# Performance work log

Hardware: AMD Instinct MI355X
Metric: run time of the kernel (lower is better)

Reference implementation:

```python
import jax, jax.numpy as jnp
import numpy as np

N_NODES = 50000
IN_CH, HID_CH, OUT_CH = 128, 128, 64
N_EDGES = 800000


def setup_inputs() -> dict:
    key = jax.random.key(0)
    k = jax.random.split(key, 6)
    x = jax.random.normal(k[0], (N_NODES, IN_CH), dtype=jnp.float32)
    edge_index = jax.random.randint(k[1], (2, N_EDGES), 0, N_NODES, dtype=jnp.int64)
    # Glorot-ish init for weights
    W1 = jax.random.normal(k[2], (IN_CH, HID_CH), dtype=jnp.float32) * (1.0 / np.sqrt(IN_CH))
    b1 = jnp.zeros((HID_CH,), dtype=jnp.float32)
    W2 = jax.random.normal(k[3], (HID_CH, OUT_CH), dtype=jnp.float32) * (1.0 / np.sqrt(HID_CH))
    b2 = jnp.zeros((OUT_CH,), dtype=jnp.float32)
    return {"x": x, "edge_index": edge_index, "W1": W1, "b1": b1, "W2": W2, "b2": b2}


def _gcn_conv(x, src, dst, W, b, n_nodes):
    """PyG GCNConv: linear, add self-loops, symmetric deg^-1/2 normalization, scatter-add."""
    h = x @ W  # [N, F_out]
    loop = jnp.arange(n_nodes, dtype=src.dtype)
    s = jnp.concatenate([src, loop])  # [E+N]
    d = jnp.concatenate([dst, loop])
    # in-degree on target nodes (including self-loops), edge weight = 1
    deg = jnp.zeros((n_nodes,), dtype=h.dtype).at[d].add(1.0)
    dinv = jnp.where(deg > 0, jax.lax.rsqrt(deg), 0.0)
    norm = dinv[s] * dinv[d]  # [E+N]
    msg = h[s] * norm[:, None]  # [E+N, F_out]
    out = jax.ops.segment_sum(msg, d, num_segments=n_nodes)
    return out + b


def reference(x, edge_index, W1, b1, W2, b2):
    src, dst = edge_index[0], edge_index[1]
    h = _gcn_conv(x, src, dst, W1, b1, N_NODES)
    h = jax.nn.relu(h)
    # dropout in eval mode -> identity
    out = _gcn_conv(h, src, dst, W2, b2, N_NODES)
    return out
```

## Files before the change

kernel.cpp:

```cpp
#include <hip/hip_runtime.h>

typedef __attribute__((ext_vector_type(8))) short bf16x8;
typedef __attribute__((ext_vector_type(4))) float f32x4;

constexpr int NN = 50000;
constexpr int NE = 800000;
constexpr int C1 = 128;
constexpr int C2 = 64;
constexpr int NBK = 196;
constexpr int EPB = 2048;
constexpr int NBLK = (NE + EPB - 1) / EPB;
constexpr int MT = NN / 16;
constexpr int MMB = 500;
constexpr int MMWAVES = MMB * 4;
constexpr int CAP = 8192;
constexpr int GB = (NN + 3) / 4;

__device__ __forceinline__ unsigned short f2bf(float f) {
    unsigned int u = __float_as_uint(f);
    u += 0x7FFFu + ((u >> 16) & 1u);
    return (unsigned short)(u >> 16);
}
__device__ __forceinline__ float2 bf2f(unsigned int u) {
    return make_float2(__uint_as_float(u << 16), __uint_as_float(u & 0xFFFF0000u));
}
__device__ __forceinline__ bf16x8 pack8(float4 a, float4 b) {
    bf16x8 r;
    r[0] = (short)f2bf(a.x); r[1] = (short)f2bf(a.y);
    r[2] = (short)f2bf(a.z); r[3] = (short)f2bf(a.w);
    r[4] = (short)f2bf(b.x); r[5] = (short)f2bf(b.y);
    r[6] = (short)f2bf(b.z); r[7] = (short)f2bf(b.w);
    return r;
}

__global__ __launch_bounds__(256) void bin_kernel(const int* __restrict__ src,
                                                  const int* __restrict__ dst,
                                                  unsigned int* __restrict__ ebuf,
                                                  int* __restrict__ localOff) {
    __shared__ int lhist[NBK];
    __shared__ int ls[256];
    __shared__ int lcur[NBK];
    __shared__ unsigned int lbuf[EPB];
    const int t = threadIdx.x;
    const int base = blockIdx.x * EPB;
    if (t < NBK) lhist[t] = 0;
    __syncthreads();
    int b[8]; unsigned int p[8];
    #pragma unroll
    for (int i = 0; i < 8; i++) {
        int e = base + i * 256 + t;
        if (e < NE) {
            int s = src[e], d = dst[e];
            b[i] = d >> 8;
            p[i] = ((unsigned int)(d & 255) << 16) | (unsigned int)s;
            atomicAdd(&lhist[b[i]], 1);
        } else b[i] = -1;
    }
    __syncthreads();
    int v = (t < NBK) ? lhist[t] : 0;
    ls[t] = v;
    __syncthreads();
    #pragma unroll
    for (int d = 1; d < 256; d <<= 1) {
        int u = (t >= d) ? ls[t - d] : 0;
        __syncthreads();
        ls[t] += u;
        __syncthreads();
    }
    if (t < NBK) {
        lcur[t] = ls[t] - v;
        localOff[blockIdx.x * 200 + t] = ls[t] - v;
    }
    if (t == NBK - 1) localOff[blockIdx.x * 200 + NBK] = ls[t];
    __syncthreads();
    #pragma unroll
    for (int i = 0; i < 8; i++) {
        if (b[i] >= 0) {
            int lp = atomicAdd(&lcur[b[i]], 1);
            lbuf[lp] = p[i];
        }
    }
    __syncthreads();
    #pragma unroll
    for (int i = 0; i < 8; i++)
        ebuf[base + i * 256 + t] = lbuf[i * 256 + t];
}

__global__ __launch_bounds__(256) void place_kernel(const unsigned int* __restrict__ ebuf,
                                                    const int* __restrict__ localOff,
                                                    unsigned short* __restrict__ esrc,
                                                    int* __restrict__ cnt,
                                                    int* __restrict__ off,
                                                    float* __restrict__ dinv) {
    __shared__ unsigned int lbuf[CAP];
    __shared__ int lhist[256];
    __shared__ int ls[256];
    __shared__ int lcur[256];
    __shared__ int red[256];
    const int t = threadIdx.x;
    const int bkt = blockIdx.x;
    const int node0 = bkt << 8;
    const int nnodes = min(256, NN - node0);

    const int j0 = 2 * t, j1 = 2 * t + 1;
    int s0 = 0, l0 = 0, s1 = 0, l1 = 0;
    if (j0 < NBLK) { s0 = localOff[j0 * 200 + bkt]; l0 = localOff[j0 * 200 + bkt + 1] - s0; }
    if (j1 < NBLK) { s1 = localOff[j1 * 200 + bkt]; l1 = localOff[j1 * 200 + bkt + 1] - s1; }

    red[t] = s0 + s1;
    ls[t] = l0 + l1;
    lhist[t] = 0;
    __syncthreads();
    #pragma unroll
    for (int d = 1; d < 256; d <<= 1) {
        int u = (t >= d) ? ls[t - d] : 0;
        int r = (t + d < 256) ? red[t + d] : 0;
        __syncthreads();
        ls[t] += u;
        red[t] += r;
        __syncthreads();
    }
    const int segBase = red[0];
    const int total = ls[255];
    const int base0 = ls[t] - (l0 + l1);
    const int base1 = base0 + l0;
    const bool fits = (total <= CAP);

    if (fits) {
        const unsigned int* q0 = ebuf + j0 * EPB + s0;
        for (int k = 0; k < l0; k++) lbuf[base0 + k] = q0[k];
        const unsigned int* q1 = ebuf + j1 * EPB + s1;
        for (int k = 0; k < l1; k++) lbuf[base1 + k] = q1[k];
        __syncthreads();
        for (int k = t; k < total; k += 256) atomicAdd(&lhist[lbuf[k] >> 16], 1);
    } else {
        const unsigned int* q0 = ebuf + j0 * EPB + s0;
        for (int k = 0; k < l0; k++) atomicAdd(&lhist[q0[k] >> 16], 1);
        const unsigned int* q1 = ebuf + j1 * EPB + s1;
        for (int k = 0; k < l1; k++) atomicAdd(&lhist[q1[k] >> 16], 1);
    }
    __syncthreads();
    int v = lhist[t];
    ls[t] = v;
    __syncthreads();
    #pragma unroll
    for (int d = 1; d < 256; d <<= 1) {
        int u = (t >= d) ? ls[t - d] : 0;
        __syncthreads();
        ls[t] += u;
        __syncthreads();
    }
    int ex = ls[t] - v;
    lcur[t] = ex;
    if (t < nnodes) {
        cnt[node0 + t] = v;
        off[node0 + t] = segBase + ex;
        dinv[node0 + t] = rsqrtf((float)v + 1.0f);
    }
    __syncthreads();
    if (fits) {
        for (int k = t; k < total; k += 256) {
            unsigned int pp = lbuf[k];
            int lp = atomicAdd(&lcur[pp >> 16], 1);
            esrc[segBase + lp] = (unsigned short)(pp & 0xFFFFu);
        }
    } else {
        const unsigned int* q0 = ebuf + j0 * EPB + s0;
        for (int k = 0; k < l0; k++) {
            unsigned int pp = q0[k];
            int lp = atomicAdd(&lcur[pp >> 16], 1);
            esrc[segBase + lp] = (unsigned short)(pp & 0xFFFFu);
        }
        const unsigned int* q1 = ebuf + j1 * EPB + s1;
        for (int k = 0; k < l1; k++) {
            unsigned int pp = q1[k];
            int lp = atomicAdd(&lcur[pp >> 16], 1);
            esrc[segBase + lp] = (unsigned short)(pp & 0xFFFFu);
        }
    }
}

__global__ __launch_bounds__(256, 2) void mm1_kernel(const float* __restrict__ x,
                                                     const float* __restrict__ W,
                                                     const float* __restrict__ dinv,
                                                     unsigned short* __restrict__ g1) {
    __shared__ unsigned short wl[4][8][64][8];
    const int t = threadIdx.x;
    for (int i = 0; i < 64; i++) {
        int idx = i * 256 + t;
        int k = idx >> 7, n = idx & 127;
        wl[k >> 5][n >> 4][((k >> 3) & 3) * 16 + (n & 15)][k & 7] = f2bf(W[idx]);
    }
    __syncthreads();
    const int lane = t & 63, lm = lane & 15, quad = lane >> 4;

    bf16x8 bfr[4][8];
    #pragma unroll
    for (int s = 0; s < 4; s++)
        #pragma unroll
        for (int nt = 0; nt < 8; nt++)
            bfr[s][nt] = *(const bf16x8*)&wl[s][nt][lane][0];

    int wg = blockIdx.x * 4 + (t >> 6);
    for (int tile = wg; tile < MT; tile += MMWAVES) {
        int row0 = tile << 4;
        const float* xr = x + (size_t)(row0 + lm) * 128 + quad * 8;
        bf16x8 af[4];
        #pragma unroll
        for (int s = 0; s < 4; s++) {
            float4 p = *(const float4*)(xr + s * 32);
            float4 q = *(const float4*)(xr + s * 32 + 4);
            af[s] = pack8(p, q);
        }
        f32x4 acc[8];
        #pragma unroll
        for (int nt = 0; nt < 8; nt++) acc[nt] = (f32x4){0.f, 0.f, 0.f, 0.f};
        #pragma unroll
        for (int s = 0; s < 4; s++)
            #pragma unroll
            for (int nt = 0; nt < 8; nt++)
                acc[nt] = __builtin_amdgcn_mfma_f32_16x16x32_bf16(af[s], bfr[s][nt],
                                                                  acc[nt], 0, 0, 0);
        float4 dv = *(const float4*)(dinv + row0 + quad * 4);
        float dvv[4] = {dv.x, dv.y, dv.z, dv.w};
        #pragma unroll
        for (int nt = 0; nt < 8; nt++)
            #pragma unroll
            for (int r = 0; r < 4; r++)
                g1[(size_t)(row0 + quad * 4 + r) * 128 + nt * 16 + lm] =
                    f2bf(acc[nt][r] * dvv[r]);
    }
}

__global__ __launch_bounds__(256, 2) void mm2_kernel(const unsigned short* __restrict__ x2,
                                                     const float* __restrict__ W,
                                                     const float* __restrict__ dinv,
                                                     unsigned short* __restrict__ g2) {
    __shared__ unsigned short wl[4][4][64][8];
    const int t = threadIdx.x;
    for (int i = 0; i < 32; i++) {
        int idx = i * 256 + t;
        int k = idx >> 6, n = idx & 63;
        wl[k >> 5][n >> 4][((k >> 3) & 3) * 16 + (n & 15)][k & 7] = f2bf(W[idx]);
    }
    __syncthreads();
    const int lane = t & 63, lm = lane & 15, quad = lane >> 4;

    bf16x8 bfr[4][4];
    #pragma unroll
    for (int s = 0; s < 4; s++)
        #pragma unroll
        for (int nt = 0; nt < 4; nt++)
            bfr[s][nt] = *(const bf16x8*)&wl[s][nt][lane][0];

    int wg = blockIdx.x * 4 + (t >> 6);
    for (int tile = wg; tile < MT; tile += MMWAVES) {
        int row0 = tile << 4;
        const bf16x8* xr = (const bf16x8*)(x2 + (size_t)(row0 + lm) * 128 + quad * 8);
        bf16x8 af[4];
        #pragma unroll
        for (int s = 0; s < 4; s++) af[s] = xr[s * 4];
        f32x4 acc[4];
        #pragma unroll
        for (int nt = 0; nt < 4; nt++) acc[nt] = (f32x4){0.f, 0.f, 0.f, 0.f};
        #pragma unroll
        for (int s = 0; s < 4; s++)
            #pragma unroll
            for (int nt = 0; nt < 4; nt++)
                acc[nt] = __builtin_amdgcn_mfma_f32_16x16x32_bf16(af[s], bfr[s][nt],
                                                                  acc[nt], 0, 0, 0);
        float4 dv = *(const float4*)(dinv + row0 + quad * 4);
        float dvv[4] = {dv.x, dv.y, dv.z, dv.w};
        #pragma unroll
        for (int nt = 0; nt < 4; nt++)
            #pragma unroll
            for (int r = 0; r < 4; r++)
                g2[(size_t)(row0 + quad * 4 + r) * 64 + nt * 16 + lm] =
                    f2bf(acc[nt][r] * dvv[r]);
    }
}

__global__ __launch_bounds__(256) void gather1_kernel(const unsigned short* __restrict__ g1,
                                                      const unsigned short* __restrict__ esrc,
                                                      const int* __restrict__ off,
                                                      const int* __restrict__ cnt,
                                                      const float* __restrict__ dinv,
                                                      const float* __restrict__ b1,
                                                      unsigned short* __restrict__ x2) {
    const int n = blockIdx.x * 4 + (threadIdx.x >> 6);
    if (n >= NN) return;
    const int lane = threadIdx.x & 63;
    const unsigned int* G = (const unsigned int*)g1;
    float2 ps = bf2f(G[(size_t)n * 64 + lane]);
    float a0 = ps.x, a1 = ps.y;
    float c0 = 0.f, c1 = 0.f;
    const int s0 = off[n], c = cnt[n];
    for (int base = 0; base < c; base += 64) {
        const int m = min(64, c - base);
        int vidx = 0;
        if (lane < m) vidx = esrc[s0 + base + lane];
        int i = 0;
        for (; i + 3 < m; i += 4) {
            int sA = __shfl(vidx, i);
            int sB = __shfl(vidx, i + 1);
            int sC = __shfl(vidx, i + 2);
            int sD = __shfl(vidx, i + 3);
            unsigned int vA = G[(size_t)sA * 64 + lane];
            unsigned int vB = G[(size_t)sB * 64 + lane];
            unsigned int vC = G[(size_t)sC * 64 + lane];
            unsigned int vD = G[(size_t)sD * 64 + lane];
            float2 pA = bf2f(vA); a0 += pA.x; a1 += pA.y;
            float2 pB = bf2f(vB); c0 += pB.x; c1 += pB.y;
            float2 pC = bf2f(vC); a0 += pC.x; a1 += pC.y;
            float2 pD = bf2f(vD); c0 += pD.x; c1 += pD.y;
        }
        for (; i < m; i++) {
            int sA = __shfl(vidx, i);
            float2 pA = bf2f(G[(size_t)sA * 64 + lane]);
            a0 += pA.x; a1 += pA.y;
        }
    }
    a0 += c0; a1 += c1;
    const float sc = dinv[n];
    const float2 bb = ((const float2*)b1)[lane];
    const float o0 = fmaxf(sc * a0 + bb.x, 0.f);
    const float o1 = fmaxf(sc * a1 + bb.y, 0.f);
    const unsigned int uo = (unsigned int)f2bf(o0) | ((unsigned int)f2bf(o1) << 16);
    ((unsigned int*)x2)[(size_t)n * 64 + lane] = uo;
}

__global__ __launch_bounds__(256) void gather2_kernel(const unsigned short* __restrict__ g2,
                                                      const unsigned short* __restrict__ esrc,
                                                      const int* __restrict__ off,
                                                      const int* __restrict__ cnt,
                                                      const float* __restrict__ dinv,
                                                      const float* __restrict__ b2,
                                                      float* __restrict__ out) {
    const int n = blockIdx.x * 4 + (threadIdx.x >> 6);
    if (n >= NN) return;
    const int lane = threadIdx.x & 63;
    const unsigned short* G = g2;
    float a0 = __uint_as_float((unsigned int)G[(size_t)n * 64 + lane] << 16);
    float c0 = 0.f;
    const int s0 = off[n], c = cnt[n];
    for (int base = 0; base < c; base += 64) {
        const int m = min(64, c - base);
        int vidx = 0;
        if (lane < m) vidx = esrc[s0 + base + lane];
        int i = 0;
        for (; i + 3 < m; i += 4) {
            int sA = __shfl(vidx, i);
            int sB = __shfl(vidx, i + 1);
            int sC = __shfl(vidx, i + 2);
            int sD = __shfl(vidx, i + 3);
            unsigned short vA = G[(size_t)sA * 64 + lane];
            unsigned short vB = G[(size_t)sB * 64 + lane];
            unsigned short vC = G[(size_t)sC * 64 + lane];
            unsigned short vD = G[(size_t)sD * 64 + lane];
            a0 += __uint_as_float((unsigned int)vA << 16);
            c0 += __uint_as_float((unsigned int)vB << 16);
            a0 += __uint_as_float((unsigned int)vC << 16);
            c0 += __uint_as_float((unsigned int)vD << 16);
        }
        for (; i < m; i++) {
            int sA = __shfl(vidx, i);
            a0 += __uint_as_float((unsigned int)G[(size_t)sA * 64 + lane] << 16);
        }
    }
    a0 += c0;
    const float sc = dinv[n];
    out[(size_t)n * 64 + lane] = sc * a0 + b2[lane];
}

extern "C" void kernel_launch(void* const* d_in, const int* in_sizes, int n_in,
                              void* d_out, int out_size, void* d_ws, size_t ws_size,
                              hipStream_t stream) {
    const float* x  = (const float*)d_in[0];
    const int* edges = (const int*)d_in[1];
    const float* W1 = (const float*)d_in[2];
    const float* b1 = (const float*)d_in[3];
    const float* W2 = (const float*)d_in[4];
    const float* b2 = (const float*)d_in[5];
    const int* src = edges;
    const int* dst = edges + NE;

    int* localOff  = (int*)d_ws;
    unsigned int* ebuf = (unsigned int*)(localOff + 78208);
    unsigned short* esrc = (unsigned short*)(ebuf + (size_t)NBLK * EPB);
    int* cnt       = (int*)(esrc + 800768);
    int* off       = cnt + 50048;
    float* dinv    = (float*)(off + 50048);
    unsigned short* g1 = (unsigned short*)(dinv + 50048);
    unsigned short* x2 = g1 + (size_t)NN * C1;
    unsigned short* g2 = g1;
    float* out = (float*)d_out;

    bin_kernel<<<NBLK, 256, 0, stream>>>(src, dst, ebuf, localOff);
    place_kernel<<<NBK, 256, 0, stream>>>(ebuf, localOff, esrc, cnt, off, dinv);

    mm1_kernel<<<MMB, 256, 0, stream>>>(x, W1, dinv, g1);
    gather1_kernel<<<GB, 256, 0, stream>>>(g1, esrc, off, cnt, dinv, b1, x2);

    mm2_kernel<<<MMB, 256, 0, stream>>>(x2, W2, dinv, g2);
    gather2_kernel<<<GB, 256, 0, stream>>>(g2, esrc, off, cnt, dinv, b2, out);
}
```

Baseline: 182.8 us.

## Fuse edge binning with first matmul and gather1 with second matmul

The edge-binning kernel and the first dense matmul now run as one horizontally fused launch, with block index deciding the role, so the matmul no longer waits for binning. The dinv row scaling of g1 moves into place_kernel, which rescales its bucket's rows after computing degrees. The first-layer gather, bias and ReLU are fused with the second matmul: each block aggregates 16 rows into shared memory and feeds them straight to MFMA, which avoids writing and rereading the x2 intermediate and drops two launches. The cost is an extra read-modify-write pass over g1 and less gather parallelism per block in the fused kernel.

```diff
diff --git a/kernel.cpp b/kernel.cpp
--- a/kernel.cpp
+++ b/kernel.cpp
@@ -11,10 +11,12 @@
 constexpr int EPB = 2048;
 constexpr int NBLK = (NE + EPB - 1) / EPB;
 constexpr int MT = NN / 16;
-constexpr int MMB = 500;
-constexpr int MMWAVES = MMB * 4;
 constexpr int CAP = 8192;
 constexpr int GB = (NN + 3) / 4;
+
+constexpr int K1G = 1024;
+constexpr int MM1_NW = (K1G - NBLK) * 4;
+constexpr int K3G = 1792;
 
 __device__ __forceinline__ unsigned short f2bf(float f) {
     unsigned int u = __float_as_uint(f);
@@ -23,6 +25,9 @@
 }
 __device__ __forceinline__ float2 bf2f(unsigned int u) {
     return make_float2(__uint_as_float(u << 16), __uint_as_float(u & 0xFFFF0000u));
+}
+__device__ __forceinline__ unsigned int pk2(float a, float b) {
+    return (unsigned int)f2bf(a) | ((unsigned int)f2bf(b) << 16);
 }
 __device__ __forceinline__ bf16x8 pack8(float4 a, float4 b) {
     bf16x8 r;
@@ -33,17 +38,19 @@
     return r;
 }
 
-__global__ __launch_bounds__(256) void bin_kernel(const int* __restrict__ src,
-                                                  const int* __restrict__ dst,
-                                                  unsigned int* __restrict__ ebuf,
-                                                  int* __restrict__ localOff) {
-    __shared__ int lhist[NBK];
-    __shared__ int ls[256];
-    __shared__ int lcur[NBK];
-    __shared__ unsigned int lbuf[EPB];
+struct BinSmem {
+    int lhist[NBK];
+    int ls[256];
+    int lcur[NBK];
+    unsigned int lbuf[EPB];
+};
+
+__device__ void bin_work(const int* __restrict__ src, const int* __restrict__ dst,
+                         unsigned int* __restrict__ ebuf, int* __restrict__ localOff,
+                         BinSmem& S) {
     const int t = threadIdx.x;
     const int base = blockIdx.x * EPB;
-    if (t < NBK) lhist[t] = 0;
+    if (t < NBK) S.lhist[t] = 0;
     __syncthreads();
     int b[8]; unsigned int p[8];
     #pragma unroll
@@ -53,37 +60,96 @@
             int s = src[e], d = dst[e];
             b[i] = d >> 8;
             p[i] = ((unsigned int)(d & 255) << 16) | (unsigned int)s;
-            atomicAdd(&lhist[b[i]], 1);
+            atomicAdd(&S.lhist[b[i]], 1);
         } else b[i] = -1;
     }
     __syncthreads();
-    int v = (t < NBK) ? lhist[t] : 0;
-    ls[t] = v;
+    int v = (t < NBK) ? S.lhist[t] : 0;
+    S.ls[t] = v;
     __syncthreads();
     #pragma unroll
     for (int d = 1; d < 256; d <<= 1) {
-        int u = (t >= d) ? ls[t - d] : 0;
-        __syncthreads();
-        ls[t] += u;
+        int u = (t >= d) ? S.ls[t - d] : 0;
+        __syncthreads();
+        S.ls[t] += u;
         __syncthreads();
     }
     if (t < NBK) {
-        lcur[t] = ls[t] - v;
-        localOff[blockIdx.x * 200 + t] = ls[t] - v;
-    }
-    if (t == NBK - 1) localOff[blockIdx.x * 200 + NBK] = ls[t];
+        S.lcur[t] = S.ls[t] - v;
+        localOff[blockIdx.x * 200 + t] = S.ls[t] - v;
+    }
+    if (t == NBK - 1) localOff[blockIdx.x * 200 + NBK] = S.ls[t];
     __syncthreads();
     #pragma unroll
     for (int i = 0; i < 8; i++) {
         if (b[i] >= 0) {
-            int lp = atomicAdd(&lcur[b[i]], 1);
-            lbuf[lp] = p[i];
+            int lp = atomicAdd(&S.lcur[b[i]], 1);
+            S.lbuf[lp] = p[i];
         }
     }
     __syncthreads();
     #pragma unroll
     for (int i = 0; i < 8; i++)
-        ebuf[base + i * 256 + t] = lbuf[i * 256 + t];
+        ebuf[base + i * 256 + t] = S.lbuf[i * 256 + t];
+}
+
+__device__ void mm1_work(const float* __restrict__ x, const float* __restrict__ W,
+                         unsigned short* __restrict__ g1,
+                         unsigned short (&wl)[4][8][64][8]) {
+    const int t = threadIdx.x;
+    for (int i = 0; i < 64; i++) {
+        int idx = i * 256 + t;
+        int k = idx >> 7, n = idx & 127;
+        wl[k >> 5][n >> 4][((k >> 3) & 3) * 16 + (n & 15)][k & 7] = f2bf(W[idx]);
+    }
+    __syncthreads();
+    const int lane = t & 63, lm = lane & 15, quad = lane >> 4;
+
+    bf16x8 bfr[4][8];
+    #pragma unroll
+    for (int s = 0; s < 4; s++)
+        #pragma unroll
+        for (int nt = 0; nt < 8; nt++)
+            bfr[s][nt] = *(const bf16x8*)&wl[s][nt][lane][0];
+
+    const int widx = (blockIdx.x - NBLK) * 4 + (t >> 6);
+    for (int tile = widx; tile < MT; tile += MM1_NW) {
+        int row0 = tile << 4;
+        const float* xr = x + (size_t)(row0 + lm) * 128 + quad * 8;
+        bf16x8 af[4];
+        #pragma unroll
+        for (int s = 0; s < 4; s++) {
+            float4 p = *(const float4*)(xr + s * 32);
+            float4 q = *(const float4*)(xr + s * 32 + 4);
+            af[s] = pack8(p, q);
+        }
+        f32x4 acc[8];
+        #pragma unroll
+        for (int nt = 0; nt < 8; nt++) acc[nt] = (f32x4){0.f, 0.f, 0.f, 0.f};
+        #pragma unroll
+        for (int s = 0; s < 4; s++)
+            #pragma unroll
+            for (int nt = 0; nt < 8; nt++)
+                acc[nt] = __builtin_amdgcn_mfma_f32_16x16x32_bf16(af[s], bfr[s][nt],
+                                                                  acc[nt], 0, 0, 0);
+        #pragma unroll
+        for (int nt = 0; nt < 8; nt++)
+            #pragma unroll
+            for (int r = 0; r < 4; r++)
+                g1[(size_t)(row0 + quad * 4 + r) * 128 + nt * 16 + lm] = f2bf(acc[nt][r]);
+    }
+}
+
+__global__ __launch_bounds__(256, 2) void k1_kernel(const int* __restrict__ src,
+                                                    const int* __restrict__ dst,
+                                                    unsigned int* __restrict__ ebuf,
+                                                    int* __restrict__ localOff,
+                                                    const float* __restrict__ x,
+                                                    const float* __restrict__ W1,
+                                                    unsigned short* __restrict__ g1) {
+    __shared__ union { BinSmem b; unsigned short wl[4][8][64][8]; } sm;
+    if (blockIdx.x < NBLK) bin_work(src, dst, ebuf, localOff, sm.b);
+    else                   mm1_work(x, W1, g1, sm.wl);
 }
 
 __global__ __launch_bounds__(256) void place_kernel(const unsigned int* __restrict__ ebuf,
@@ -91,7 +157,8 @@
                                                     unsigned short* __restrict__ esrc,
                                                     int* __restrict__ cnt,
                                                     int* __restrict__ off,
-                                                    float* __restrict__ dinv) {
+                                                    float* __restrict__ dinv,
+                                                    unsigned short* __restrict__ g1) {
     __shared__ unsigned int lbuf[CAP];
     __shared__ int lhist[256];
     __shared__ int ls[256];
@@ -178,155 +245,92 @@
             esrc[segBase + lp] = (unsigned short)(pp & 0xFFFFu);
         }
     }
-}
-
-__global__ __launch_bounds__(256, 2) void mm1_kernel(const float* __restrict__ x,
-                                                     const float* __restrict__ W,
-                                                     const float* __restrict__ dinv,
-                                                     unsigned short* __restrict__ g1) {
-    __shared__ unsigned short wl[4][8][64][8];
-    const int t = threadIdx.x;
-    for (int i = 0; i < 64; i++) {
-        int idx = i * 256 + t;
-        int k = idx >> 7, n = idx & 127;
-        wl[k >> 5][n >> 4][((k >> 3) & 3) * 16 + (n & 15)][k & 7] = f2bf(W[idx]);
-    }
-    __syncthreads();
-    const int lane = t & 63, lm = lane & 15, quad = lane >> 4;
-
-    bf16x8 bfr[4][8];
-    #pragma unroll
-    for (int s = 0; s < 4; s++)
-        #pragma unroll
-        for (int nt = 0; nt < 8; nt++)
-            bfr[s][nt] = *(const bf16x8*)&wl[s][nt][lane][0];
-
-    int wg = blockIdx.x * 4 + (t >> 6);
-    for (int tile = wg; tile < MT; tile += MMWAVES) {
-        int row0 = tile << 4;
-        const float* xr = x + (size_t)(row0 + lm) * 128 + quad * 8;
-        bf16x8 af[4];
-        #pragma unroll
-        for (int s = 0; s < 4; s++) {
-            float4 p = *(const float4*)(xr + s * 32);
-            float4 q = *(const float4*)(xr + s * 32 + 4);
-            af[s] = pack8(p, q);
-        }
-        f32x4 acc[8];
-        #pragma unroll
-        for (int nt = 0; nt < 8; nt++) acc[nt] = (f32x4){0.f, 0.f, 0.f, 0.f};
-        #pragma unroll
-        for (int s = 0; s < 4; s++)
-            #pragma unroll
-            for (int nt = 0; nt < 8; nt++)
-                acc[nt] = __builtin_amdgcn_mfma_f32_16x16x32_bf16(af[s], bfr[s][nt],
-                                                                  acc[nt], 0, 0, 0);
-        float4 dv = *(const float4*)(dinv + row0 + quad * 4);
-        float dvv[4] = {dv.x, dv.y, dv.z, dv.w};
-        #pragma unroll
-        for (int nt = 0; nt < 8; nt++)
-            #pragma unroll
-            for (int r = 0; r < 4; r++)
-                g1[(size_t)(row0 + quad * 4 + r) * 128 + nt * 16 + lm] =
-                    f2bf(acc[nt][r] * dvv[r]);
-    }
-}
-
-__global__ __launch_bounds__(256, 2) void mm2_kernel(const unsigned short* __restrict__ x2,
-                                                     const float* __restrict__ W,
-                                                     const float* __restrict__ dinv,
-                                                     unsigned short* __restrict__ g2) {
-    __shared__ unsigned short wl[4][4][64][8];
+    const int w = t >> 6, lane = t & 63;
+    unsigned int* g1u = (unsigned int*)g1;
+    for (int r = w; r < nnodes; r += 4) {
+        const float dn = dinv[node0 + r];
+        const size_t a = (size_t)(node0 + r) * 64 + lane;
+        float2 p = bf2f(g1u[a]);
+        g1u[a] = pk2(dn * p.x, dn * p.y);
+    }
+}
+
+__global__ __launch_bounds__(256) void gmm_kernel(const unsigned short* __restrict__ g1,
+                                                  const unsigned short* __restrict__ esrc,
+                                                  const int* __restrict__ off,
+                                                  const int* __restrict__ cnt,
+                                                  const float* __restrict__ dinv,
+                                                  const float* __restrict__ b1,
+                                                  const float* __restrict__ W2,
+                                                  unsigned short* __restrict__ g2) {
+    __shared__ unsigned short wl2[4][4][64][8];
+    __shared__ unsigned short x2t[16][136];
     const int t = threadIdx.x;
     for (int i = 0; i < 32; i++) {
         int idx = i * 256 + t;
         int k = idx >> 6, n = idx & 63;
-        wl[k >> 5][n >> 4][((k >> 3) & 3) * 16 + (n & 15)][k & 7] = f2bf(W[idx]);
-    }
-    __syncthreads();
-    const int lane = t & 63, lm = lane & 15, quad = lane >> 4;
-
-    bf16x8 bfr[4][4];
-    #pragma unroll
-    for (int s = 0; s < 4; s++)
-        #pragma unroll
-        for (int nt = 0; nt < 4; nt++)
-            bfr[s][nt] = *(const bf16x8*)&wl[s][nt][lane][0];
-
-    int wg = blockIdx.x * 4 + (t >> 6);
-    for (int tile = wg; tile < MT; tile += MMWAVES) {
-        int row0 = tile << 4;
-        const bf16x8* xr = (const bf16x8*)(x2 + (size_t)(row0 + lm) * 128 + quad * 8);
+        wl2[k >> 5][n >> 4][((k >> 3) & 3) * 16 + (n & 15)][k & 7] = f2bf(W2[idx]);
+    }
+    const int lane = t & 63, w = t >> 6, lm = lane & 15, quad = lane >> 4;
+    const unsigned int* G = (const unsigned int*)g1;
+    const float2 bb = ((const float2*)b1)[lane];
+
+    for (int tile = blockIdx.x; tile < MT; tile += K3G) {
+        __syncthreads();
+        #pragma unroll 1
+        for (int k4 = 0; k4 < 4; k4++) {
+            const int n = tile * 16 + w * 4 + k4;
+            float2 ps = bf2f(G[(size_t)n * 64 + lane]);
+            float a0 = ps.x, a1 = ps.y;
+            float c0 = 0.f, c1 = 0.f;
+            const int s0 = off[n], c = cnt[n];
+            for (int base = 0; base < c; base += 64) {
+                const int m = min(64, c - base);
+                int vidx = 0;
+                if (lane < m) vidx = esrc[s0 + base + lane];
+                int i = 0;
+                for (; i + 3 < m; i += 4) {
+                    int sA = __shfl(vidx, i),     sB = __shfl(vidx, i + 1);
+                    int sC = __shfl(vidx, i + 2), sD = __shfl(vidx, i + 3);
+                    unsigned int vA = G[(size_t)sA * 64 + lane];
+                    unsigned int vB = G[(size_t)sB * 64 + lane];
+                    unsigned int vC = G[(size_t)sC * 64 + lane];
+                    unsigned int vD = G[(size_t)sD * 64 + lane];
+                    float2 pA = bf2f(vA); a0 += pA.x; a1 += pA.y;
+                    float2 pB = bf2f(vB); c0 += pB.x; c1 += pB.y;
+                    float2 pC = bf2f(vC); a0 += pC.x; a1 += pC.y;
+                    float2 pD = bf2f(vD); c0 += pD.x; c1 += pD.y;
+                }
+                for (; i < m; i++) {
+                    int sA = __shfl(vidx, i);
+                    float2 pA = bf2f(G[(size_t)sA * 64 + lane]);
+                    a0 += pA.x; a1 += pA.y;
+                }
+            }
+            a0 += c0; a1 += c1;
+            const float sc = dinv[n];
+            const float o0 = fmaxf(sc * a0 + bb.x, 0.f);
+            const float o1 = fmaxf(sc * a1 + bb.y, 0.f);
+            ((unsigned int*)&x2t[w * 4 + k4][0])[lane] = pk2(o0, o1);
+        }
+        __syncthreads();
+        const int row0 = tile << 4;
         bf16x8 af[4];
         #pragma unroll
-        for (int s = 0; s < 4; s++) af[s] = xr[s * 4];
-        f32x4 acc[4];
-        #pragma unroll
-        for (int nt = 0; nt < 4; nt++) acc[nt] = (f32x4){0.f, 0.f, 0.f, 0.f};
-        #pragma unroll
         for (int s = 0; s < 4; s++)
-            #pragma unroll
-            for (int nt = 0; nt < 4; nt++)
-                acc[nt] = __builtin_amdgcn_mfma_f32_16x16x32_bf16(af[s], bfr[s][nt],
-                                                                  acc[nt], 0, 0, 0);
+            af[s] = *(const bf16x8*)&x2t[lm][quad * 8 + s * 32];
+        f32x4 acc = (f32x4){0.f, 0.f, 0.f, 0.f};
+        #pragma unroll
+        for (int s = 0; s < 4; s++) {
+            bf16x8 bfr = *(const bf16x8*)&wl2[s][w][lane][0];
+            acc = __builtin_amdgcn_mfma_f32_16x16x32_bf16(af[s], bfr, acc, 0, 0, 0);
+        }
         float4 dv = *(const float4*)(dinv + row0 + quad * 4);
         float dvv[4] = {dv.x, dv.y, dv.z, dv.w};
         #pragma unroll
-        for (int nt = 0; nt < 4; nt++)
-            #pragma unroll
-            for (int r = 0; r < 4; r++)
-                g2[(size_t)(row0 + quad * 4 + r) * 64 + nt * 16 + lm] =
-                    f2bf(acc[nt][r] * dvv[r]);
-    }
-}
-
-__global__ __launch_bounds__(256) void gather1_kernel(const unsigned short* __restrict__ g1,
-                                                      const unsigned short* __restrict__ esrc,
-                                                      const int* __restrict__ off,
-                                                      const int* __restrict__ cnt,
-                                                      const float* __restrict__ dinv,
-                                                      const float* __restrict__ b1,
-                                                      unsigned short* __restrict__ x2) {
-    const int n = blockIdx.x * 4 + (threadIdx.x >> 6);
-    if (n >= NN) return;
-    const int lane = threadIdx.x & 63;
-    const unsigned int* G = (const unsigned int*)g1;
-    float2 ps = bf2f(G[(size_t)n * 64 + lane]);
-    float a0 = ps.x, a1 = ps.y;
-    float c0 = 0.f, c1 = 0.f;
-    const int s0 = off[n], c = cnt[n];
-    for (int base = 0; base < c; base += 64) {
-        const int m = min(64, c - base);
-        int vidx = 0;
-        if (lane < m) vidx = esrc[s0 + base + lane];
-        int i = 0;
-        for (; i + 3 < m; i += 4) {
-            int sA = __shfl(vidx, i);
-            int sB = __shfl(vidx, i + 1);
-            int sC = __shfl(vidx, i + 2);
-            int sD = __shfl(vidx, i + 3);
-            unsigned int vA = G[(size_t)sA * 64 + lane];
-            unsigned int vB = G[(size_t)sB * 64 + lane];
-            unsigned int vC = G[(size_t)sC * 64 + lane];
-            unsigned int vD = G[(size_t)sD * 64 + lane];
-            float2 pA = bf2f(vA); a0 += pA.x; a1 += pA.y;
-            float2 pB = bf2f(vB); c0 += pB.x; c1 += pB.y;
-            float2 pC = bf2f(vC); a0 += pC.x; a1 += pC.y;
-            float2 pD = bf2f(vD); c0 += pD.x; c1 += pD.y;
-        }
-        for (; i < m; i++) {
-            int sA = __shfl(vidx, i);
-            float2 pA = bf2f(G[(size_t)sA * 64 + lane]);
-            a0 += pA.x; a1 += pA.y;
-        }
-    }
-    a0 += c0; a1 += c1;
-    const float sc = dinv[n];
-    const float2 bb = ((const float2*)b1)[lane];
-    const float o0 = fmaxf(sc * a0 + bb.x, 0.f);
-    const float o1 = fmaxf(sc * a1 + bb.y, 0.f);
-    const unsigned int uo = (unsigned int)f2bf(o0) | ((unsigned int)f2bf(o1) << 16);
-    ((unsigned int*)x2)[(size_t)n * 64 + lane] = uo;
+        for (int r = 0; r < 4; r++)
+            g2[(size_t)(row0 + quad * 4 + r) * 64 + w * 16 + lm] = f2bf(acc[r] * dvv[r]);
+    }
 }
 
 __global__ __launch_bounds__(256) void gather2_kernel(const unsigned short* __restrict__ g2,
@@ -349,10 +353,8 @@
         if (lane < m) vidx = esrc[s0 + base + lane];
         int i = 0;
         for (; i + 3 < m; i += 4) {
-            int sA = __shfl(vidx, i);
-            int sB = __shfl(vidx, i + 1);
-            int sC = __shfl(vidx, i + 2);
-            int sD = __shfl(vidx, i + 3);
+            int sA = __shfl(vidx, i),     sB = __shfl(vidx, i + 1);
+            int sC = __shfl(vidx, i + 2), sD = __shfl(vidx, i + 3);
             unsigned short vA = G[(size_t)sA * 64 + lane];
             unsigned short vB = G[(size_t)sB * 64 + lane];
             unsigned short vC = G[(size_t)sC * 64 + lane];
@@ -368,8 +370,7 @@
         }
     }
     a0 += c0;
-    const float sc = dinv[n];
-    out[(size_t)n * 64 + lane] = sc * a0 + b2[lane];
+    out[(size_t)n * 64 + lane] = dinv[n] * a0 + b2[lane];
 }
 
 extern "C" void kernel_launch(void* const* d_in, const int* in_sizes, int n_in,
@@ -391,16 +392,11 @@
     int* off       = cnt + 50048;
     float* dinv    = (float*)(off + 50048);
     unsigned short* g1 = (unsigned short*)(dinv + 50048);
-    unsigned short* x2 = g1 + (size_t)NN * C1;
-    unsigned short* g2 = g1;
+    unsigned short* g2 = g1 + (size_t)NN * C1;
     float* out = (float*)d_out;
 
-    bin_kernel<<<NBLK, 256, 0, stream>>>(src, dst, ebuf, localOff);
-    place_kernel<<<NBK, 256, 0, stream>>>(ebuf, localOff, esrc, cnt, off, dinv);
-
-    mm1_kernel<<<MMB, 256, 0, stream>>>(x, W1, dinv, g1);
-    gather1_kernel<<<GB, 256, 0, stream>>>(g1, esrc, off, cnt, dinv, b1, x2);
-
-    mm2_kernel<<<MMB, 256, 0, stream>>>(x2, W2, dinv, g2);
+    k1_kernel<<<K1G, 256, 0, stream>>>(src, dst, ebuf, localOff, x, W1, g1);
+    place_kernel<<<NBK, 256, 0, stream>>>(ebuf, localOff, esrc, cnt, off, dinv, g1);
+    gmm_kernel<<<K3G, 256, 0, stream>>>(g1, esrc, off, cnt, dinv, b1, W2, g2);
     gather2_kernel<<<GB, 256, 0, stream>>>(g2, esrc, off, cnt, dinv, b2, out);
 }
```

New measurement: 188.4 us. 1.03x slower.
